# Performance work log

Hardware: AMD Instinct MI355X
Metric: run time of the kernel (lower is better)

## Reference

```python
import jax, jax.numpy as jnp
import numpy as np

N = 50000
E = 600000
D_IN = 128
D_OUT = 128
EPS = 1e-12  # F.normalize eps


def setup_inputs() -> dict:
    key = jax.random.key(0)
    ks = jax.random.split(key, 10)
    s = 1.0 / np.sqrt(D_IN)
    inp = {
        "x": jax.random.normal(ks[0], (N, D_IN), dtype=jnp.float32),
        "edge_index": jax.random.randint(ks[1], (2, E), 0, N, dtype=jnp.int64),
        # conv1: lin_l (with bias) applied to aggregated neighbors, lin_r (no bias) to root
        "W1l": jax.random.uniform(ks[2], (D_IN, D_IN), jnp.float32, -s, s),
        "b1": jax.random.uniform(ks[3], (D_IN,), jnp.float32, -s, s),
        "W1r": jax.random.uniform(ks[4], (D_IN, D_IN), jnp.float32, -s, s),
        # conv2
        "W2l": jax.random.uniform(ks[5], (D_IN, D_OUT), jnp.float32, -s, s),
        "b2": jax.random.uniform(ks[6], (D_OUT,), jnp.float32, -s, s),
        "W2r": jax.random.uniform(ks[7], (D_IN, D_OUT), jnp.float32, -s, s),
        # final fc
        "Wf": jax.random.uniform(ks[8], (D_OUT, D_OUT), jnp.float32, -s, s),
        "bf": jax.random.uniform(ks[9], (D_OUT,), jnp.float32, -s, s),
    }
    return inp


def _sage_conv(x, src, dst, Wl, bl, Wr):
    # mean-aggregate messages from source nodes onto destination nodes
    msgs = x[src]  # [E, d] gather
    agg = jax.ops.segment_sum(msgs, dst, num_segments=N)  # [N, d]
    cnt = jax.ops.segment_sum(jnp.ones((src.shape[0],), x.dtype), dst, num_segments=N)
    agg = agg / jnp.maximum(cnt, 1.0)[:, None]  # isolated nodes -> 0
    out = agg @ Wl + bl + x @ Wr
    # L2 normalize per node (PyG normalize=True)
    nrm = jnp.sqrt(jnp.sum(out * out, axis=-1, keepdims=True))
    return out / jnp.maximum(nrm, EPS)


def reference(x, edge_index, W1l, b1, W1r, W2l, b2, W2r, Wf, bf):
    src, dst = edge_index[0], edge_index[1]
    h = jax.nn.relu(_sage_conv(x, src, dst, W1l, b1, W1r))
    h = jax.nn.relu(_sage_conv(h, src, dst, W2l, b2, W2r))
    return h @ Wf + bf
```

## Files before the change

kernel.cpp:

```cpp
#include <hip/hip_runtime.h>
#include <hip/hip_fp16.h>

#define D 128
#define SCAN_B 256
#define HLD 136

typedef __attribute__((ext_vector_type(8))) _Float16 f16x8;
typedef __attribute__((ext_vector_type(4))) float f32x4;

__global__ void count_kernel(const int* __restrict__ ei, int E, int* __restrict__ cnt) {
    int t = blockIdx.x * blockDim.x + threadIdx.x;
    if (t < E) atomicAdd(&cnt[ei[E + t]], 1);
}

__global__ void scan_pass1(const int* __restrict__ cnt, int* __restrict__ rs,
                           int* __restrict__ bsum, int N) {
    __shared__ int lds[SCAN_B];
    int tid = threadIdx.x;
    int i = blockIdx.x * SCAN_B + tid;
    int v = (i < N) ? cnt[i] : 0;
    lds[tid] = v;
    __syncthreads();
    for (int o = 1; o < SCAN_B; o <<= 1) {
        int t = (tid >= o) ? lds[tid - o] : 0;
        __syncthreads();
        lds[tid] += t;
        __syncthreads();
    }
    if (i < N) rs[i] = lds[tid] - v;
    if (tid == SCAN_B - 1) bsum[blockIdx.x] = lds[tid];
}

__global__ void scan_pass2(int* __restrict__ bsum, int nb) {
    __shared__ int lds[SCAN_B];
    int tid = threadIdx.x;
    int v = (tid < nb) ? bsum[tid] : 0;
    lds[tid] = v;
    __syncthreads();
    for (int o = 1; o < SCAN_B; o <<= 1) {
        int t = (tid >= o) ? lds[tid - o] : 0;
        __syncthreads();
        lds[tid] += t;
        __syncthreads();
    }
    if (tid < nb) bsum[tid] = lds[tid] - v;
}

__global__ void scan_pass3(int* __restrict__ rs, int* __restrict__ cursor,
                           const int* __restrict__ bsum, const int* __restrict__ cnt,
                           float* __restrict__ inv, int N) {
    int i = blockIdx.x * SCAN_B + threadIdx.x;
    if (i < N) {
        int v = rs[i] + bsum[blockIdx.x];
        rs[i] = v;
        cursor[i] = v;
        inv[i] = 1.0f / (float)max(cnt[i], 1);
    }
}

__global__ void fill_kernel(const int* __restrict__ ei, int E,
                            int* __restrict__ cursor, int* __restrict__ csr) {
    int e = blockIdx.x * blockDim.x + threadIdx.x;
    if (e < E) {
        int src = ei[e], dst = ei[E + e];
        int pos = atomicAdd(&cursor[dst], 1);
        csr[pos] = src;
    }
}

__global__ void cvt_half_kernel(const float* __restrict__ x, __half* __restrict__ xh, int n8) {
    int i = blockIdx.x * blockDim.x + threadIdx.x;
    if (i >= n8) return;
    const float4* x4 = (const float4*)x;
    float4 a = x4[2 * i], b = x4[2 * i + 1];
    __half2 h0 = __floats2half2_rn(a.x, a.y);
    __half2 h1 = __floats2half2_rn(a.z, a.w);
    __half2 h2 = __floats2half2_rn(b.x, b.y);
    __half2 h3 = __floats2half2_rn(b.z, b.w);
    uint4 o;
    o.x = *(const unsigned*)&h0;
    o.y = *(const unsigned*)&h1;
    o.z = *(const unsigned*)&h2;
    o.w = *(const unsigned*)&h3;
    ((uint4*)xh)[i] = o;
}

__device__ __forceinline__ void acc8(uint4 v, float* s) {
    const __half2* h = reinterpret_cast<const __half2*>(&v);
    float2 f0 = __half22float2(h[0]);
    float2 f1 = __half22float2(h[1]);
    float2 f2 = __half22float2(h[2]);
    float2 f3 = __half22float2(h[3]);
    s[0] += f0.x; s[1] += f0.y; s[2] += f1.x; s[3] += f1.y;
    s[4] += f2.x; s[5] += f2.y; s[6] += f3.x; s[7] += f3.y;
}

__global__ void aggregate_kernel(const __half* __restrict__ xh, int sstride,
                                 const int* __restrict__ csr,
                                 const int* __restrict__ rs, const int* __restrict__ cnt,
                                 const float* __restrict__ inv,
                                 __half* __restrict__ aggh, __half* __restrict__ aggl, int N) {
    int t = blockIdx.x * blockDim.x + threadIdx.x;
    int node = t >> 4;
    int c = t & 15;
    if (node >= N) return;
    int deg = cnt[node];
    int st = rs[node];
    const uint4* x4 = (const uint4*)xh;
    float s[8] = {0.f, 0.f, 0.f, 0.f, 0.f, 0.f, 0.f, 0.f};
    int i = 0;
    for (; i + 4 <= deg; i += 4) {
        int n0 = csr[st + i + 0], n1 = csr[st + i + 1];
        int n2 = csr[st + i + 2], n3 = csr[st + i + 3];
        uint4 v0 = x4[(size_t)n0 * sstride + c];
        uint4 v1 = x4[(size_t)n1 * sstride + c];
        uint4 v2 = x4[(size_t)n2 * sstride + c];
        uint4 v3 = x4[(size_t)n3 * sstride + c];
        acc8(v0, s); acc8(v1, s); acc8(v2, s); acc8(v3, s);
    }
    for (; i < deg; i++) {
        int n0 = csr[st + i];
        uint4 v0 = x4[(size_t)n0 * sstride + c];
        acc8(v0, s);
    }
    float iv = inv[node];
    uint4 oh, ol;
    __half2* ph = (__half2*)&oh;
    __half2* pl = (__half2*)&ol;
#pragma unroll
    for (int jj = 0; jj < 4; jj++) {
        float v0 = s[2 * jj] * iv, v1 = s[2 * jj + 1] * iv;
        __half h0 = __float2half_rn(v0), h1 = __float2half_rn(v1);
        ph[jj] = __halves2half2(h0, h1);
        pl[jj] = __halves2half2(__float2half_rn(v0 - __half2float(h0)),
                                __float2half_rn(v1 - __half2float(h1)));
    }
    ((uint4*)aggh)[(size_t)node * 16 + c] = oh;
    ((uint4*)aggl)[(size_t)node * 16 + c] = ol;
}

__global__ void pack_kernel(const float* __restrict__ W1l, const float* __restrict__ W1r,
                            const float* __restrict__ W2l, const float* __restrict__ W2r,
                            const float* __restrict__ Wf, unsigned short* __restrict__ pw) {
    int idx = blockIdx.x * blockDim.x + threadIdx.x;
    if (idx >= 5 * 2048) return;
    int w = idx >> 11;
    int r = idx & 2047;
    int ks = r >> 9;
    int t = (r >> 6) & 7;
    int lane = r & 63;
    int q = lane >> 4, n = lane & 15;
    const float* W = (w == 0) ? W1l : (w == 1) ? W1r : (w == 2) ? W2l : (w == 3) ? W2r : Wf;
    unsigned short* dh = pw + (size_t)w * 32768;
    unsigned short* dl = dh + 16384;
    int off = ((ks * 8 + t) * 64 + lane) * 8;
#pragma unroll
    for (int j = 0; j < 8; j++) {
        float v = W[(size_t)(ks * 32 + q * 8 + j) * D + t * 16 + n];
        __half hb = __float2half_rn(v);
        dh[off + j] = __half_as_ushort(hb);
        dl[off + j] = __half_as_ushort(__float2half_rn(v - __half2float(hb)));
    }
}

__device__ __forceinline__ void split_f16(const float* v, uint4& hi, uint4& lo) {
    __half2* ph = (__half2*)&hi;
    __half2* pl = (__half2*)&lo;
#pragma unroll
    for (int jj = 0; jj < 4; jj++) {
        __half h0 = __float2half_rn(v[2 * jj]);
        __half h1 = __float2half_rn(v[2 * jj + 1]);
        ph[jj] = __halves2half2(h0, h1);
        pl[jj] = __halves2half2(__float2half_rn(v[2 * jj] - __half2float(h0)),
                                __float2half_rn(v[2 * jj + 1] - __half2float(h1)));
    }
}

template <int LAYER>
__global__ __launch_bounds__(256) void mfma_gemm(
        const uint4* __restrict__ Agh, const uint4* __restrict__ Agl,
        const float* __restrict__ Xf,
        const uint4* Hio,
        const uint4* __restrict__ W0h, const uint4* __restrict__ W0l,
        const uint4* __restrict__ W1h, const uint4* __restrict__ W1l,
        const float* __restrict__ bias,
        const uint4* __restrict__ W2h, const uint4* __restrict__ W2l,
        const float* __restrict__ bias2,
        float* out, __half* Hout, int N) {
    __shared__ __half Hs[(LAYER == 2) ? 4 * 2 * 16 * HLD : 4];

    const int tid = threadIdx.x;
    const int lane = tid & 63;
    const int wave = tid >> 6;
    const int c = lane & 15;
    const int q = lane >> 4;
    const int R = blockIdx.x * 64 + wave * 16;
    int row0 = R + c;
    if (row0 >= N) row0 = N - 1;

    uint4 Ah_[8], Al_[8];
    const size_t rb16 = (size_t)row0 * 16 + q;
#pragma unroll
    for (int kl = 0; kl < 4; kl++) {
        Ah_[kl] = Agh[rb16 + kl * 4];
        Al_[kl] = Agl[rb16 + kl * 4];
    }
    if (LAYER == 1) {
        const float4* xf4 = (const float4*)Xf;
        const size_t xb = (size_t)row0 * 32 + q * 2;
        float4 xa[8];
#pragma unroll
        for (int kl = 0; kl < 4; kl++) {
            xa[2 * kl] = xf4[xb + kl * 8];
            xa[2 * kl + 1] = xf4[xb + kl * 8 + 1];
        }
#pragma unroll
        for (int kl = 0; kl < 4; kl++) {
            float v[8] = {xa[2 * kl].x, xa[2 * kl].y, xa[2 * kl].z, xa[2 * kl].w,
                          xa[2 * kl + 1].x, xa[2 * kl + 1].y, xa[2 * kl + 1].z, xa[2 * kl + 1].w};
            split_f16(v, Ah_[4 + kl], Al_[4 + kl]);
        }
    } else {
        const size_t rb32 = (size_t)row0 * 32 + q;
#pragma unroll
        for (int kl = 0; kl < 4; kl++) {
            Ah_[4 + kl] = Hio[rb32 + kl * 4];
            Al_[4 + kl] = Hio[rb32 + 16 + kl * 4];
        }
    }

    f32x4 acc[8];
#pragma unroll
    for (int t = 0; t < 8; t++)
#pragma unroll
        for (int r = 0; r < 4; r++) acc[t][r] = 0.0f;

#pragma unroll
    for (int ks = 0; ks < 8; ks++) {
        const uint4* Wh = ((ks < 4) ? W0h : W1h) + (size_t)(ks & 3) * 512 + lane;
        const uint4* Wl = ((ks < 4) ? W0l : W1l) + (size_t)(ks & 3) * 512 + lane;
        f16x8 ah = __builtin_bit_cast(f16x8, Ah_[ks]);
        f16x8 al = __builtin_bit_cast(f16x8, Al_[ks]);
#pragma unroll
        for (int t = 0; t < 8; t++) {
            f16x8 bh = __builtin_bit_cast(f16x8, Wh[t * 64]);
            f16x8 bl = __builtin_bit_cast(f16x8, Wl[t * 64]);
            acc[t] = __builtin_amdgcn_mfma_f32_16x16x32_f16(ah, bh, acc[t], 0, 0, 0);
            acc[t] = __builtin_amdgcn_mfma_f32_16x16x32_f16(al, bh, acc[t], 0, 0, 0);
            acc[t] = __builtin_amdgcn_mfma_f32_16x16x32_f16(ah, bl, acc[t], 0, 0, 0);
        }
    }

#pragma unroll
    for (int t = 0; t < 8; t++) {
        float bv = bias[t * 16 + c];
#pragma unroll
        for (int r = 0; r < 4; r++) acc[t][r] += bv;
    }
#pragma unroll
    for (int r = 0; r < 4; r++) {
        float v = 0.0f;
#pragma unroll
        for (int t = 0; t < 8; t++) v += acc[t][r] * acc[t][r];
        v += __shfl_xor(v, 1, 16);
        v += __shfl_xor(v, 2, 16);
        v += __shfl_xor(v, 4, 16);
        v += __shfl_xor(v, 8, 16);
        float rn = 1.0f / fmaxf(sqrtf(v), 1e-12f);
#pragma unroll
        for (int t = 0; t < 8; t++) acc[t][r] = fmaxf(acc[t][r] * rn, 0.0f);
    }

    if (LAYER == 1) {
#pragma unroll
        for (int t = 0; t < 8; t++)
#pragma unroll
            for (int r = 0; r < 4; r++) {
                int row = R + q * 4 + r;
                if (row < N) {
                    float v = acc[t][r];
                    __half h = __float2half_rn(v);
                    size_t base = (size_t)row * 256;
                    Hout[base + t * 16 + c] = h;
                    Hout[base + 128 + t * 16 + c] = __float2half_rn(v - __half2float(h));
                }
            }
        return;
    }

    __half* hh = &Hs[wave * (2 * 16 * HLD)];
    __half* hl = hh + 16 * HLD;
#pragma unroll
    for (int t = 0; t < 8; t++)
#pragma unroll
        for (int r = 0; r < 4; r++) {
            int m = q * 4 + r;
            float v = acc[t][r];
            __half h = __float2half_rn(v);
            hh[m * HLD + t * 16 + c] = h;
            hl[m * HLD + t * 16 + c] = __float2half_rn(v - __half2float(h));
        }
    __syncthreads();

    uint4 a2h_[4], a2l_[4];
#pragma unroll
    for (int k2 = 0; k2 < 4; k2++) {
        a2h_[k2] = *(const uint4*)&hh[c * HLD + k2 * 32 + q * 8];
        a2l_[k2] = *(const uint4*)&hl[c * HLD + k2 * 32 + q * 8];
    }

    f32x4 acc2[8];
#pragma unroll
    for (int t = 0; t < 8; t++) {
        float bv = bias2[t * 16 + c];
#pragma unroll
        for (int r = 0; r < 4; r++) acc2[t][r] = bv;
    }
#pragma unroll
    for (int k2 = 0; k2 < 4; k2++) {
        const uint4* Wh = W2h + (size_t)k2 * 512 + lane;
        const uint4* Wl = W2l + (size_t)k2 * 512 + lane;
        f16x8 ah = __builtin_bit_cast(f16x8, a2h_[k2]);
        f16x8 al = __builtin_bit_cast(f16x8, a2l_[k2]);
#pragma unroll
        for (int t = 0; t < 8; t++) {
            f16x8 bh = __builtin_bit_cast(f16x8, Wh[t * 64]);
            f16x8 bl = __builtin_bit_cast(f16x8, Wl[t * 64]);
            acc2[t] = __builtin_amdgcn_mfma_f32_16x16x32_f16(ah, bh, acc2[t], 0, 0, 0);
            acc2[t] = __builtin_amdgcn_mfma_f32_16x16x32_f16(al, bh, acc2[t], 0, 0, 0);
            acc2[t] = __builtin_amdgcn_mfma_f32_16x16x32_f16(ah, bl, acc2[t], 0, 0, 0);
        }
    }

#pragma unroll
    for (int t = 0; t < 8; t++)
#pragma unroll
        for (int r = 0; r < 4; r++) {
            int row = R + q * 4 + r;
            if (row < N) out[(size_t)row * D + t * 16 + c] = acc2[t][r];
        }
}

extern "C" void kernel_launch(void* const* d_in, const int* in_sizes, int n_in,
                              void* d_out, int out_size, void* d_ws, size_t ws_size,
                              hipStream_t stream) {
    const float* x   = (const float*)d_in[0];
    const int*   ei  = (const int*)d_in[1];
    const float* W1l = (const float*)d_in[2];
    const float* b1  = (const float*)d_in[3];
    const float* W1r = (const float*)d_in[4];
    const float* W2l = (const float*)d_in[5];
    const float* b2  = (const float*)d_in[6];
    const float* W2r = (const float*)d_in[7];
    const float* Wf  = (const float*)d_in[8];
    const float* bf  = (const float*)d_in[9];
    float* out = (float*)d_out;

    int N = in_sizes[0] / D;
    int E = in_sizes[1] / 2;

    __half* Agh = (__half*)d_ws;
    __half* Agl = Agh + (size_t)N * D;
    __half* Xh  = Agl + (size_t)N * D;
    float* inv  = (float*)(Xh + (size_t)N * D);
    int*   rs     = (int*)(inv + N);
    int*   cnt    = rs + N;
    int*   cursor = cnt + N;
    int*   bsum   = cursor + N;
    int*   csr    = bsum + 256;
    unsigned short* pw = (unsigned short*)(csr + E);
    unsigned short* p1lh = pw + 0 * 32768, *p1ll = p1lh + 16384;
    unsigned short* p1rh = pw + 1 * 32768, *p1rl = p1rh + 16384;
    unsigned short* p2lh = pw + 2 * 32768, *p2ll = p2lh + 16384;
    unsigned short* p2rh = pw + 3 * 32768, *p2rl = p2rh + 16384;
    unsigned short* pfh  = pw + 4 * 32768, *pfl  = pfh + 16384;

    __half* H1 = (__half*)d_out;

    int nb = (N + SCAN_B - 1) / SCAN_B;

    hipMemsetAsync(cnt, 0, (size_t)N * sizeof(int), stream);
    pack_kernel<<<40, 256, 0, stream>>>(W1l, W1r, W2l, W2r, Wf, pw);
    int n8 = N * 16;
    cvt_half_kernel<<<(n8 + 255) / 256, 256, 0, stream>>>(x, Xh, n8);
    count_kernel<<<(E + 255) / 256, 256, 0, stream>>>(ei, E, cnt);
    scan_pass1<<<nb, SCAN_B, 0, stream>>>(cnt, rs, bsum, N);
    scan_pass2<<<1, SCAN_B, 0, stream>>>(bsum, nb);
    scan_pass3<<<nb, SCAN_B, 0, stream>>>(rs, cursor, bsum, cnt, inv, N);
    fill_kernel<<<(E + 255) / 256, 256, 0, stream>>>(ei, E, cursor, csr);

    int agg_blocks = (N * 16 + 255) / 256;
    int gemm_blocks = (N + 63) / 64;

    aggregate_kernel<<<agg_blocks, 256, 0, stream>>>(Xh, 16, csr, rs, cnt, inv, Agh, Agl, N);
    mfma_gemm<1><<<gemm_blocks, 256, 0, stream>>>(
        (const uint4*)Agh, (const uint4*)Agl, x, nullptr,
        (const uint4*)p1lh, (const uint4*)p1ll, (const uint4*)p1rh, (const uint4*)p1rl, b1,
        nullptr, nullptr, nullptr, nullptr, H1, N);

    aggregate_kernel<<<agg_blocks, 256, 0, stream>>>(H1, 32, csr, rs, cnt, inv, Agh, Agl, N);
    mfma_gemm<2><<<gemm_blocks, 256, 0, stream>>>(
        (const uint4*)Agh, (const uint4*)Agl, nullptr, (const uint4*)d_out,
        (const uint4*)p2lh, (const uint4*)p2ll, (const uint4*)p2rh, (const uint4*)p2rl, b2,
        (const uint4*)pfh, (const uint4*)pfl, bf, out, nullptr, N);
}
```

Baseline: 280.5 us.

## Fuse prologue kernels and process two row tiles per wave in MFMA GEMM

Merges weight packing, x-to-half conversion and in-degree counting into one prologue launch, which removes two kernel launches and their serialization gaps. The GEMM kernels now have each wave compute two 16-row tiles, so every weight fragment loaded from global memory feeds twice as many MFMAs, and the grid is halved. The cost is roughly double the register use for the A fragments and accumulators; launch_bounds(256,2) caps registers to keep occupancy and may cause spills. Layer 2 also reuses the shared-memory staging buffer once per tile, which adds barriers.

```diff
diff --git a/kernel.cpp b/kernel.cpp
--- a/kernel.cpp
+++ b/kernel.cpp
@@ -7,11 +7,6 @@
 
 typedef __attribute__((ext_vector_type(8))) _Float16 f16x8;
 typedef __attribute__((ext_vector_type(4))) float f32x4;
-
-__global__ void count_kernel(const int* __restrict__ ei, int E, int* __restrict__ cnt) {
-    int t = blockIdx.x * blockDim.x + threadIdx.x;
-    if (t < E) atomicAdd(&cnt[ei[E + t]], 1);
-}
 
 __global__ void scan_pass1(const int* __restrict__ cnt, int* __restrict__ rs,
                            int* __restrict__ bsum, int N) {
@@ -68,21 +63,49 @@
     }
 }
 
-__global__ void cvt_half_kernel(const float* __restrict__ x, __half* __restrict__ xh, int n8) {
-    int i = blockIdx.x * blockDim.x + threadIdx.x;
-    if (i >= n8) return;
-    const float4* x4 = (const float4*)x;
-    float4 a = x4[2 * i], b = x4[2 * i + 1];
-    __half2 h0 = __floats2half2_rn(a.x, a.y);
-    __half2 h1 = __floats2half2_rn(a.z, a.w);
-    __half2 h2 = __floats2half2_rn(b.x, b.y);
-    __half2 h3 = __floats2half2_rn(b.z, b.w);
-    uint4 o;
-    o.x = *(const unsigned*)&h0;
-    o.y = *(const unsigned*)&h1;
-    o.z = *(const unsigned*)&h2;
-    o.w = *(const unsigned*)&h3;
-    ((uint4*)xh)[i] = o;
+__global__ void prologue_kernel(const float* __restrict__ W1l, const float* __restrict__ W1r,
+                                const float* __restrict__ W2l, const float* __restrict__ W2r,
+                                const float* __restrict__ Wf, unsigned short* __restrict__ pw,
+                                const float* __restrict__ x, __half* __restrict__ xh, int n8,
+                                const int* __restrict__ ei, int E, int* __restrict__ cnt) {
+    int t = blockIdx.x * blockDim.x + threadIdx.x;
+    if (t < 10240) {
+        int idx = t;
+        int w = idx >> 11;
+        int r = idx & 2047;
+        int ks = r >> 9;
+        int tt = (r >> 6) & 7;
+        int lane = r & 63;
+        int q = lane >> 4, n = lane & 15;
+        const float* W = (w == 0) ? W1l : (w == 1) ? W1r : (w == 2) ? W2l : (w == 3) ? W2r : Wf;
+        unsigned short* dh = pw + (size_t)w * 32768;
+        unsigned short* dl = dh + 16384;
+        int off = ((ks * 8 + tt) * 64 + lane) * 8;
+#pragma unroll
+        for (int j = 0; j < 8; j++) {
+            float v = W[(size_t)(ks * 32 + q * 8 + j) * D + tt * 16 + n];
+            __half hb = __float2half_rn(v);
+            dh[off + j] = __half_as_ushort(hb);
+            dl[off + j] = __half_as_ushort(__float2half_rn(v - __half2float(hb)));
+        }
+    } else if (t < 10240 + n8) {
+        int i = t - 10240;
+        const float4* x4 = (const float4*)x;
+        float4 a = x4[2 * i], b = x4[2 * i + 1];
+        __half2 h0 = __floats2half2_rn(a.x, a.y);
+        __half2 h1 = __floats2half2_rn(a.z, a.w);
+        __half2 h2 = __floats2half2_rn(b.x, b.y);
+        __half2 h3 = __floats2half2_rn(b.z, b.w);
+        uint4 o;
+        o.x = *(const unsigned*)&h0;
+        o.y = *(const unsigned*)&h1;
+        o.z = *(const unsigned*)&h2;
+        o.w = *(const unsigned*)&h3;
+        ((uint4*)xh)[i] = o;
+    } else {
+        int e = t - 10240 - n8;
+        if (e < E) atomicAdd(&cnt[ei[E + e]], 1);
+    }
 }
 
 __device__ __forceinline__ void acc8(uint4 v, float* s) {
@@ -139,30 +162,6 @@
     ((uint4*)aggl)[(size_t)node * 16 + c] = ol;
 }
 
-__global__ void pack_kernel(const float* __restrict__ W1l, const float* __restrict__ W1r,
-                            const float* __restrict__ W2l, const float* __restrict__ W2r,
-                            const float* __restrict__ Wf, unsigned short* __restrict__ pw) {
-    int idx = blockIdx.x * blockDim.x + threadIdx.x;
-    if (idx >= 5 * 2048) return;
-    int w = idx >> 11;
-    int r = idx & 2047;
-    int ks = r >> 9;
-    int t = (r >> 6) & 7;
-    int lane = r & 63;
-    int q = lane >> 4, n = lane & 15;
-    const float* W = (w == 0) ? W1l : (w == 1) ? W1r : (w == 2) ? W2l : (w == 3) ? W2r : Wf;
-    unsigned short* dh = pw + (size_t)w * 32768;
-    unsigned short* dl = dh + 16384;
-    int off = ((ks * 8 + t) * 64 + lane) * 8;
-#pragma unroll
-    for (int j = 0; j < 8; j++) {
-        float v = W[(size_t)(ks * 32 + q * 8 + j) * D + t * 16 + n];
-        __half hb = __float2half_rn(v);
-        dh[off + j] = __half_as_ushort(hb);
-        dl[off + j] = __half_as_ushort(__float2half_rn(v - __half2float(hb)));
-    }
-}
-
 __device__ __forceinline__ void split_f16(const float* v, uint4& hi, uint4& lo) {
     __half2* ph = (__half2*)&hi;
     __half2* pl = (__half2*)&lo;
@@ -177,7 +176,7 @@
 }
 
 template <int LAYER>
-__global__ __launch_bounds__(256) void mfma_gemm(
+__global__ __launch_bounds__(256, 2) void mfma_gemm(
         const uint4* __restrict__ Agh, const uint4* __restrict__ Agl,
         const float* __restrict__ Xf,
         const uint4* Hio,
@@ -194,151 +193,175 @@
     const int wave = tid >> 6;
     const int c = lane & 15;
     const int q = lane >> 4;
-    const int R = blockIdx.x * 64 + wave * 16;
-    int row0 = R + c;
-    if (row0 >= N) row0 = N - 1;
-
-    uint4 Ah_[8], Al_[8];
-    const size_t rb16 = (size_t)row0 * 16 + q;
-#pragma unroll
-    for (int kl = 0; kl < 4; kl++) {
-        Ah_[kl] = Agh[rb16 + kl * 4];
-        Al_[kl] = Agl[rb16 + kl * 4];
-    }
-    if (LAYER == 1) {
-        const float4* xf4 = (const float4*)Xf;
-        const size_t xb = (size_t)row0 * 32 + q * 2;
-        float4 xa[8];
+    const int R = blockIdx.x * 128 + wave * 32;
+
+    int rowA[2];
+    rowA[0] = min(R + c, N - 1);
+    rowA[1] = min(R + 16 + c, N - 1);
+
+    uint4 Ah_[2][8], Al_[2][8];
+#pragma unroll
+    for (int tile = 0; tile < 2; tile++) {
+        const size_t rb16 = (size_t)rowA[tile] * 16 + q;
 #pragma unroll
         for (int kl = 0; kl < 4; kl++) {
-            xa[2 * kl] = xf4[xb + kl * 8];
-            xa[2 * kl + 1] = xf4[xb + kl * 8 + 1];
-        }
-#pragma unroll
-        for (int kl = 0; kl < 4; kl++) {
-            float v[8] = {xa[2 * kl].x, xa[2 * kl].y, xa[2 * kl].z, xa[2 * kl].w,
-                          xa[2 * kl + 1].x, xa[2 * kl + 1].y, xa[2 * kl + 1].z, xa[2 * kl + 1].w};
-            split_f16(v, Ah_[4 + kl], Al_[4 + kl]);
-        }
-    } else {
-        const size_t rb32 = (size_t)row0 * 32 + q;
-#pragma unroll
-        for (int kl = 0; kl < 4; kl++) {
-            Ah_[4 + kl] = Hio[rb32 + kl * 4];
-            Al_[4 + kl] = Hio[rb32 + 16 + kl * 4];
-        }
-    }
-
-    f32x4 acc[8];
-#pragma unroll
-    for (int t = 0; t < 8; t++)
-#pragma unroll
-        for (int r = 0; r < 4; r++) acc[t][r] = 0.0f;
+            Ah_[tile][kl] = Agh[rb16 + kl * 4];
+            Al_[tile][kl] = Agl[rb16 + kl * 4];
+        }
+        if (LAYER == 1) {
+            const float4* xf4 = (const float4*)Xf;
+            const size_t xb = (size_t)rowA[tile] * 32 + q * 2;
+#pragma unroll
+            for (int kl = 0; kl < 4; kl++) {
+                float4 xa = xf4[xb + kl * 8];
+                float4 xbv = xf4[xb + kl * 8 + 1];
+                float v[8] = {xa.x, xa.y, xa.z, xa.w, xbv.x, xbv.y, xbv.z, xbv.w};
+                split_f16(v, Ah_[tile][4 + kl], Al_[tile][4 + kl]);
+            }
+        } else {
+            const size_t rb32 = (size_t)rowA[tile] * 32 + q;
+#pragma unroll
+            for (int kl = 0; kl < 4; kl++) {
+                Ah_[tile][4 + kl] = Hio[rb32 + kl * 4];
+                Al_[tile][4 + kl] = Hio[rb32 + 16 + kl * 4];
+            }
+        }
+    }
+
+    f32x4 acc[2][8];
+#pragma unroll
+    for (int tile = 0; tile < 2; tile++)
+#pragma unroll
+        for (int t = 0; t < 8; t++)
+#pragma unroll
+            for (int r = 0; r < 4; r++) acc[tile][t][r] = 0.0f;
 
 #pragma unroll
     for (int ks = 0; ks < 8; ks++) {
         const uint4* Wh = ((ks < 4) ? W0h : W1h) + (size_t)(ks & 3) * 512 + lane;
         const uint4* Wl = ((ks < 4) ? W0l : W1l) + (size_t)(ks & 3) * 512 + lane;
-        f16x8 ah = __builtin_bit_cast(f16x8, Ah_[ks]);
-        f16x8 al = __builtin_bit_cast(f16x8, Al_[ks]);
+        f16x8 a0h = __builtin_bit_cast(f16x8, Ah_[0][ks]);
+        f16x8 a0l = __builtin_bit_cast(f16x8, Al_[0][ks]);
+        f16x8 a1h = __builtin_bit_cast(f16x8, Ah_[1][ks]);
+        f16x8 a1l = __builtin_bit_cast(f16x8, Al_[1][ks]);
 #pragma unroll
         for (int t = 0; t < 8; t++) {
             f16x8 bh = __builtin_bit_cast(f16x8, Wh[t * 64]);
             f16x8 bl = __builtin_bit_cast(f16x8, Wl[t * 64]);
-            acc[t] = __builtin_amdgcn_mfma_f32_16x16x32_f16(ah, bh, acc[t], 0, 0, 0);
-            acc[t] = __builtin_amdgcn_mfma_f32_16x16x32_f16(al, bh, acc[t], 0, 0, 0);
-            acc[t] = __builtin_amdgcn_mfma_f32_16x16x32_f16(ah, bl, acc[t], 0, 0, 0);
-        }
-    }
-
-#pragma unroll
-    for (int t = 0; t < 8; t++) {
-        float bv = bias[t * 16 + c];
-#pragma unroll
-        for (int r = 0; r < 4; r++) acc[t][r] += bv;
-    }
-#pragma unroll
-    for (int r = 0; r < 4; r++) {
-        float v = 0.0f;
-#pragma unroll
-        for (int t = 0; t < 8; t++) v += acc[t][r] * acc[t][r];
-        v += __shfl_xor(v, 1, 16);
-        v += __shfl_xor(v, 2, 16);
-        v += __shfl_xor(v, 4, 16);
-        v += __shfl_xor(v, 8, 16);
-        float rn = 1.0f / fmaxf(sqrtf(v), 1e-12f);
-#pragma unroll
-        for (int t = 0; t < 8; t++) acc[t][r] = fmaxf(acc[t][r] * rn, 0.0f);
+            acc[0][t] = __builtin_amdgcn_mfma_f32_16x16x32_f16(a0h, bh, acc[0][t], 0, 0, 0);
+            acc[0][t] = __builtin_amdgcn_mfma_f32_16x16x32_f16(a0l, bh, acc[0][t], 0, 0, 0);
+            acc[0][t] = __builtin_amdgcn_mfma_f32_16x16x32_f16(a0h, bl, acc[0][t], 0, 0, 0);
+            acc[1][t] = __builtin_amdgcn_mfma_f32_16x16x32_f16(a1h, bh, acc[1][t], 0, 0, 0);
+            acc[1][t] = __builtin_amdgcn_mfma_f32_16x16x32_f16(a1l, bh, acc[1][t], 0, 0, 0);
+            acc[1][t] = __builtin_amdgcn_mfma_f32_16x16x32_f16(a1h, bl, acc[1][t], 0, 0, 0);
+        }
+    }
+
+#pragma unroll
+    for (int tile = 0; tile < 2; tile++) {
+#pragma unroll
+        for (int t = 0; t < 8; t++) {
+            float bv = bias[t * 16 + c];
+#pragma unroll
+            for (int r = 0; r < 4; r++) acc[tile][t][r] += bv;
+        }
+#pragma unroll
+        for (int r = 0; r < 4; r++) {
+            float v = 0.0f;
+#pragma unroll
+            for (int t = 0; t < 8; t++) v += acc[tile][t][r] * acc[tile][t][r];
+            v += __shfl_xor(v, 1, 16);
+            v += __shfl_xor(v, 2, 16);
+            v += __shfl_xor(v, 4, 16);
+            v += __shfl_xor(v, 8, 16);
+            float rn = 1.0f / fmaxf(sqrtf(v), 1e-12f);
+#pragma unroll
+            for (int t = 0; t < 8; t++) acc[tile][t][r] = fmaxf(acc[tile][t][r] * rn, 0.0f);
+        }
     }
 
     if (LAYER == 1) {
 #pragma unroll
-        for (int t = 0; t < 8; t++)
-#pragma unroll
-            for (int r = 0; r < 4; r++) {
-                int row = R + q * 4 + r;
-                if (row < N) {
-                    float v = acc[t][r];
-                    __half h = __float2half_rn(v);
-                    size_t base = (size_t)row * 256;
-                    Hout[base + t * 16 + c] = h;
-                    Hout[base + 128 + t * 16 + c] = __float2half_rn(v - __half2float(h));
+        for (int tile = 0; tile < 2; tile++)
+#pragma unroll
+            for (int t = 0; t < 8; t++)
+#pragma unroll
+                for (int r = 0; r < 4; r++) {
+                    int row = R + tile * 16 + q * 4 + r;
+                    if (row < N) {
+                        float v = acc[tile][t][r];
+                        __half h = __float2half_rn(v);
+                        size_t base = (size_t)row * 256;
+                        Hout[base + t * 16 + c] = h;
+                        Hout[base + 128 + t * 16 + c] = __float2half_rn(v - __half2float(h));
+                    }
                 }
-            }
         return;
     }
 
     __half* hh = &Hs[wave * (2 * 16 * HLD)];
     __half* hl = hh + 16 * HLD;
-#pragma unroll
-    for (int t = 0; t < 8; t++)
-#pragma unroll
-        for (int r = 0; r < 4; r++) {
-            int m = q * 4 + r;
-            float v = acc[t][r];
-            __half h = __float2half_rn(v);
-            hh[m * HLD + t * 16 + c] = h;
-            hl[m * HLD + t * 16 + c] = __float2half_rn(v - __half2float(h));
-        }
-    __syncthreads();
-
-    uint4 a2h_[4], a2l_[4];
-#pragma unroll
-    for (int k2 = 0; k2 < 4; k2++) {
-        a2h_[k2] = *(const uint4*)&hh[c * HLD + k2 * 32 + q * 8];
-        a2l_[k2] = *(const uint4*)&hl[c * HLD + k2 * 32 + q * 8];
-    }
-
-    f32x4 acc2[8];
-#pragma unroll
-    for (int t = 0; t < 8; t++) {
-        float bv = bias2[t * 16 + c];
-#pragma unroll
-        for (int r = 0; r < 4; r++) acc2[t][r] = bv;
-    }
+    uint4 a2h_[2][4], a2l_[2][4];
+#pragma unroll
+    for (int tile = 0; tile < 2; tile++) {
+        __syncthreads();
+#pragma unroll
+        for (int t = 0; t < 8; t++)
+#pragma unroll
+            for (int r = 0; r < 4; r++) {
+                int m = q * 4 + r;
+                float v = acc[tile][t][r];
+                __half h = __float2half_rn(v);
+                hh[m * HLD + t * 16 + c] = h;
+                hl[m * HLD + t * 16 + c] = __float2half_rn(v - __half2float(h));
+            }
+        __syncthreads();
+#pragma unroll
+        for (int k2 = 0; k2 < 4; k2++) {
+            a2h_[tile][k2] = *(const uint4*)&hh[c * HLD + k2 * 32 + q * 8];
+            a2l_[tile][k2] = *(const uint4*)&hl[c * HLD + k2 * 32 + q * 8];
+        }
+    }
+
+    f32x4 acc2[2][8];
+#pragma unroll
+    for (int tile = 0; tile < 2; tile++)
+#pragma unroll
+        for (int t = 0; t < 8; t++) {
+            float bv = bias2[t * 16 + c];
+#pragma unroll
+            for (int r = 0; r < 4; r++) acc2[tile][t][r] = bv;
+        }
 #pragma unroll
     for (int k2 = 0; k2 < 4; k2++) {
         const uint4* Wh = W2h + (size_t)k2 * 512 + lane;
         const uint4* Wl = W2l + (size_t)k2 * 512 + lane;
-        f16x8 ah = __builtin_bit_cast(f16x8, a2h_[k2]);
-        f16x8 al = __builtin_bit_cast(f16x8, a2l_[k2]);
+        f16x8 a0h = __builtin_bit_cast(f16x8, a2h_[0][k2]);
+        f16x8 a0l = __builtin_bit_cast(f16x8, a2l_[0][k2]);
+        f16x8 a1h = __builtin_bit_cast(f16x8, a2h_[1][k2]);
+        f16x8 a1l = __builtin_bit_cast(f16x8, a2l_[1][k2]);
 #pragma unroll
         for (int t = 0; t < 8; t++) {
             f16x8 bh = __builtin_bit_cast(f16x8, Wh[t * 64]);
             f16x8 bl = __builtin_bit_cast(f16x8, Wl[t * 64]);
-            acc2[t] = __builtin_amdgcn_mfma_f32_16x16x32_f16(ah, bh, acc2[t], 0, 0, 0);
-            acc2[t] = __builtin_amdgcn_mfma_f32_16x16x32_f16(al, bh, acc2[t], 0, 0, 0);
-            acc2[t] = __builtin_amdgcn_mfma_f32_16x16x32_f16(ah, bl, acc2[t], 0, 0, 0);
-        }
-    }
-
-#pragma unroll
-    for (int t = 0; t < 8; t++)
-#pragma unroll
-        for (int r = 0; r < 4; r++) {
-            int row = R + q * 4 + r;
-            if (row < N) out[(size_t)row * D + t * 16 + c] = acc2[t][r];
-        }
+            acc2[0][t] = __builtin_amdgcn_mfma_f32_16x16x32_f16(a0h, bh, acc2[0][t], 0, 0, 0);
+            acc2[0][t] = __builtin_amdgcn_mfma_f32_16x16x32_f16(a0l, bh, acc2[0][t], 0, 0, 0);
+            acc2[0][t] = __builtin_amdgcn_mfma_f32_16x16x32_f16(a0h, bl, acc2[0][t], 0, 0, 0);
+            acc2[1][t] = __builtin_amdgcn_mfma_f32_16x16x32_f16(a1h, bh, acc2[1][t], 0, 0, 0);
+            acc2[1][t] = __builtin_amdgcn_mfma_f32_16x16x32_f16(a1l, bh, acc2[1][t], 0, 0, 0);
+            acc2[1][t] = __builtin_amdgcn_mfma_f32_16x16x32_f16(a1h, bl, acc2[1][t], 0, 0, 0);
+        }
+    }
+
+#pragma unroll
+    for (int tile = 0; tile < 2; tile++)
+#pragma unroll
+        for (int t = 0; t < 8; t++)
+#pragma unroll
+            for (int r = 0; r < 4; r++) {
+                int row = R + tile * 16 + q * 4 + r;
+                if (row < N) out[(size_t)row * D + t * 16 + c] = acc2[tile][t][r];
+            }
 }
 
 extern "C" void kernel_launch(void* const* d_in, const int* in_sizes, int n_in,
@@ -378,19 +401,19 @@
     __half* H1 = (__half*)d_out;
 
     int nb = (N + SCAN_B - 1) / SCAN_B;
+    int n8 = N * 16;
 
     hipMemsetAsync(cnt, 0, (size_t)N * sizeof(int), stream);
-    pack_kernel<<<40, 256, 0, stream>>>(W1l, W1r, W2l, W2r, Wf, pw);
-    int n8 = N * 16;
-    cvt_half_kernel<<<(n8 + 255) / 256, 256, 0, stream>>>(x, Xh, n8);
-    count_kernel<<<(E + 255) / 256, 256, 0, stream>>>(ei, E, cnt);
+    int pro_threads = 10240 + n8 + E;
+    prologue_kernel<<<(pro_threads + 255) / 256, 256, 0, stream>>>(
+        W1l, W1r, W2l, W2r, Wf, pw, x, Xh, n8, ei, E, cnt);
     scan_pass1<<<nb, SCAN_B, 0, stream>>>(cnt, rs, bsum, N);
     scan_pass2<<<1, SCAN_B, 0, stream>>>(bsum, nb);
     scan_pass3<<<nb, SCAN_B, 0, stream>>>(rs, cursor, bsum, cnt, inv, N);
     fill_kernel<<<(E + 255) / 256, 256, 0, stream>>>(ei, E, cursor, csr);
 
     int agg_blocks = (N * 16 + 255) / 256;
-    int gemm_blocks = (N + 63) / 64;
+    int gemm_blocks = (N + 127) / 128;
 
     aggregate_kernel<<<agg_blocks, 256, 0, stream>>>(Xh, 16, csr, rs, cnt, inv, Agh, Agl, N);
     mfma_gemm<1><<<gemm_blocks, 256, 0, stream>>>(
```

Result: slower. 291.3 us (+3.8%).

## Fuse prologue kernels into one launch and double-buffer weight loads in GEMM

Applied to the files above, without the earlier changes.

Merges the weight packing, fp16 conversion of x and in-degree counting kernels into a single launch that partitions threads by index range, removing two kernel launches and their serialization gaps. Separately, both GEMM loops now prefetch the next K-slice of packed weights into a register double buffer before issuing the MFMAs for the current slice, aiming to hide global/L2 load latency behind matrix math. The prefetch raises register pressure (32 extra uint4 per buffer pair), which may reduce occupancy or cause spills.

```diff
diff --git a/kernel.cpp b/kernel.cpp
--- a/kernel.cpp
+++ b/kernel.cpp
@@ -7,11 +7,6 @@
 
 typedef __attribute__((ext_vector_type(8))) _Float16 f16x8;
 typedef __attribute__((ext_vector_type(4))) float f32x4;
-
-__global__ void count_kernel(const int* __restrict__ ei, int E, int* __restrict__ cnt) {
-    int t = blockIdx.x * blockDim.x + threadIdx.x;
-    if (t < E) atomicAdd(&cnt[ei[E + t]], 1);
-}
 
 __global__ void scan_pass1(const int* __restrict__ cnt, int* __restrict__ rs,
                            int* __restrict__ bsum, int N) {
@@ -68,21 +63,49 @@
     }
 }
 
-__global__ void cvt_half_kernel(const float* __restrict__ x, __half* __restrict__ xh, int n8) {
-    int i = blockIdx.x * blockDim.x + threadIdx.x;
-    if (i >= n8) return;
-    const float4* x4 = (const float4*)x;
-    float4 a = x4[2 * i], b = x4[2 * i + 1];
-    __half2 h0 = __floats2half2_rn(a.x, a.y);
-    __half2 h1 = __floats2half2_rn(a.z, a.w);
-    __half2 h2 = __floats2half2_rn(b.x, b.y);
-    __half2 h3 = __floats2half2_rn(b.z, b.w);
-    uint4 o;
-    o.x = *(const unsigned*)&h0;
-    o.y = *(const unsigned*)&h1;
-    o.z = *(const unsigned*)&h2;
-    o.w = *(const unsigned*)&h3;
-    ((uint4*)xh)[i] = o;
+__global__ void prologue_kernel(const float* __restrict__ W1l, const float* __restrict__ W1r,
+                                const float* __restrict__ W2l, const float* __restrict__ W2r,
+                                const float* __restrict__ Wf, unsigned short* __restrict__ pw,
+                                const float* __restrict__ x, __half* __restrict__ xh, int n8,
+                                const int* __restrict__ ei, int E, int* __restrict__ cnt) {
+    int t = blockIdx.x * blockDim.x + threadIdx.x;
+    if (t < 10240) {
+        int idx = t;
+        int w = idx >> 11;
+        int r = idx & 2047;
+        int ks = r >> 9;
+        int tt = (r >> 6) & 7;
+        int lane = r & 63;
+        int q = lane >> 4, n = lane & 15;
+        const float* W = (w == 0) ? W1l : (w == 1) ? W1r : (w == 2) ? W2l : (w == 3) ? W2r : Wf;
+        unsigned short* dh = pw + (size_t)w * 32768;
+        unsigned short* dl = dh + 16384;
+        int off = ((ks * 8 + tt) * 64 + lane) * 8;
+#pragma unroll
+        for (int j = 0; j < 8; j++) {
+            float v = W[(size_t)(ks * 32 + q * 8 + j) * D + tt * 16 + n];
+            __half hb = __float2half_rn(v);
+            dh[off + j] = __half_as_ushort(hb);
+            dl[off + j] = __half_as_ushort(__float2half_rn(v - __half2float(hb)));
+        }
+    } else if (t < 10240 + n8) {
+        int i = t - 10240;
+        const float4* x4 = (const float4*)x;
+        float4 a = x4[2 * i], b = x4[2 * i + 1];
+        __half2 h0 = __floats2half2_rn(a.x, a.y);
+        __half2 h1 = __floats2half2_rn(a.z, a.w);
+        __half2 h2 = __floats2half2_rn(b.x, b.y);
+        __half2 h3 = __floats2half2_rn(b.z, b.w);
+        uint4 o;
+        o.x = *(const unsigned*)&h0;
+        o.y = *(const unsigned*)&h1;
+        o.z = *(const unsigned*)&h2;
+        o.w = *(const unsigned*)&h3;
+        ((uint4*)xh)[i] = o;
+    } else {
+        int e = t - 10240 - n8;
+        if (e < E) atomicAdd(&cnt[ei[E + e]], 1);
+    }
 }
 
 __device__ __forceinline__ void acc8(uint4 v, float* s) {
@@ -139,30 +162,6 @@
     ((uint4*)aggl)[(size_t)node * 16 + c] = ol;
 }
 
-__global__ void pack_kernel(const float* __restrict__ W1l, const float* __restrict__ W1r,
-                            const float* __restrict__ W2l, const float* __restrict__ W2r,
-                            const float* __restrict__ Wf, unsigned short* __restrict__ pw) {
-    int idx = blockIdx.x * blockDim.x + threadIdx.x;
-    if (idx >= 5 * 2048) return;
-    int w = idx >> 11;
-    int r = idx & 2047;
-    int ks = r >> 9;
-    int t = (r >> 6) & 7;
-    int lane = r & 63;
-    int q = lane >> 4, n = lane & 15;
-    const float* W = (w == 0) ? W1l : (w == 1) ? W1r : (w == 2) ? W2l : (w == 3) ? W2r : Wf;
-    unsigned short* dh = pw + (size_t)w * 32768;
-    unsigned short* dl = dh + 16384;
-    int off = ((ks * 8 + t) * 64 + lane) * 8;
-#pragma unroll
-    for (int j = 0; j < 8; j++) {
-        float v = W[(size_t)(ks * 32 + q * 8 + j) * D + t * 16 + n];
-        __half hb = __float2half_rn(v);
-        dh[off + j] = __half_as_ushort(hb);
-        dl[off + j] = __half_as_ushort(__float2half_rn(v - __half2float(hb)));
-    }
-}
-
 __device__ __forceinline__ void split_f16(const float* v, uint4& hi, uint4& lo) {
     __half2* ph = (__half2*)&hi;
     __half2* pl = (__half2*)&lo;
@@ -195,8 +194,7 @@
     const int c = lane & 15;
     const int q = lane >> 4;
     const int R = blockIdx.x * 64 + wave * 16;
-    int row0 = R + c;
-    if (row0 >= N) row0 = N - 1;
+    const int row0 = min(R + c, N - 1);
 
     uint4 Ah_[8], Al_[8];
     const size_t rb16 = (size_t)row0 * 16 + q;
@@ -229,6 +227,13 @@
         }
     }
 
+    uint4 wh[2][8], wl[2][8];
+#pragma unroll
+    for (int t = 0; t < 8; t++) {
+        wh[0][t] = W0h[(size_t)t * 64 + lane];
+        wl[0][t] = W0l[(size_t)t * 64 + lane];
+    }
+
     f32x4 acc[8];
 #pragma unroll
     for (int t = 0; t < 8; t++)
@@ -237,14 +242,21 @@
 
 #pragma unroll
     for (int ks = 0; ks < 8; ks++) {
-        const uint4* Wh = ((ks < 4) ? W0h : W1h) + (size_t)(ks & 3) * 512 + lane;
-        const uint4* Wl = ((ks < 4) ? W0l : W1l) + (size_t)(ks & 3) * 512 + lane;
+        if (ks < 7) {
+            const uint4* Whn = (((ks + 1) < 4) ? W0h : W1h) + (size_t)((ks + 1) & 3) * 512 + lane;
+            const uint4* Wln = (((ks + 1) < 4) ? W0l : W1l) + (size_t)((ks + 1) & 3) * 512 + lane;
+#pragma unroll
+            for (int t = 0; t < 8; t++) {
+                wh[(ks + 1) & 1][t] = Whn[t * 64];
+                wl[(ks + 1) & 1][t] = Wln[t * 64];
+            }
+        }
         f16x8 ah = __builtin_bit_cast(f16x8, Ah_[ks]);
         f16x8 al = __builtin_bit_cast(f16x8, Al_[ks]);
 #pragma unroll
         for (int t = 0; t < 8; t++) {
-            f16x8 bh = __builtin_bit_cast(f16x8, Wh[t * 64]);
-            f16x8 bl = __builtin_bit_cast(f16x8, Wl[t * 64]);
+            f16x8 bh = __builtin_bit_cast(f16x8, wh[ks & 1][t]);
+            f16x8 bl = __builtin_bit_cast(f16x8, wl[ks & 1][t]);
             acc[t] = __builtin_amdgcn_mfma_f32_16x16x32_f16(ah, bh, acc[t], 0, 0, 0);
             acc[t] = __builtin_amdgcn_mfma_f32_16x16x32_f16(al, bh, acc[t], 0, 0, 0);
             acc[t] = __builtin_amdgcn_mfma_f32_16x16x32_f16(ah, bl, acc[t], 0, 0, 0);
@@ -288,6 +300,13 @@
         return;
     }
 
+    uint4 w2h[2][8], w2l[2][8];
+#pragma unroll
+    for (int t = 0; t < 8; t++) {
+        w2h[0][t] = W2h[(size_t)t * 64 + lane];
+        w2l[0][t] = W2l[(size_t)t * 64 + lane];
+    }
+
     __half* hh = &Hs[wave * (2 * 16 * HLD)];
     __half* hl = hh + 16 * HLD;
 #pragma unroll
@@ -318,14 +337,21 @@
     }
 #pragma unroll
     for (int k2 = 0; k2 < 4; k2++) {
-        const uint4* Wh = W2h + (size_t)k2 * 512 + lane;
-        const uint4* Wl = W2l + (size_t)k2 * 512 + lane;
+        if (k2 < 3) {
+            const uint4* Whn = W2h + (size_t)(k2 + 1) * 512 + lane;
+            const uint4* Wln = W2l + (size_t)(k2 + 1) * 512 + lane;
+#pragma unroll
+            for (int t = 0; t < 8; t++) {
+                w2h[(k2 + 1) & 1][t] = Whn[t * 64];
+                w2l[(k2 + 1) & 1][t] = Wln[t * 64];
+            }
+        }
         f16x8 ah = __builtin_bit_cast(f16x8, a2h_[k2]);
         f16x8 al = __builtin_bit_cast(f16x8, a2l_[k2]);
 #pragma unroll
         for (int t = 0; t < 8; t++) {
-            f16x8 bh = __builtin_bit_cast(f16x8, Wh[t * 64]);
-            f16x8 bl = __builtin_bit_cast(f16x8, Wl[t * 64]);
+            f16x8 bh = __builtin_bit_cast(f16x8, w2h[k2 & 1][t]);
+            f16x8 bl = __builtin_bit_cast(f16x8, w2l[k2 & 1][t]);
             acc2[t] = __builtin_amdgcn_mfma_f32_16x16x32_f16(ah, bh, acc2[t], 0, 0, 0);
             acc2[t] = __builtin_amdgcn_mfma_f32_16x16x32_f16(al, bh, acc2[t], 0, 0, 0);
             acc2[t] = __builtin_amdgcn_mfma_f32_16x16x32_f16(ah, bl, acc2[t], 0, 0, 0);
@@ -378,12 +404,12 @@
     __half* H1 = (__half*)d_out;
 
     int nb = (N + SCAN_B - 1) / SCAN_B;
+    int n8 = N * 16;
 
     hipMemsetAsync(cnt, 0, (size_t)N * sizeof(int), stream);
-    pack_kernel<<<40, 256, 0, stream>>>(W1l, W1r, W2l, W2r, Wf, pw);
-    int n8 = N * 16;
-    cvt_half_kernel<<<(n8 + 255) / 256, 256, 0, stream>>>(x, Xh, n8);
-    count_kernel<<<(E + 255) / 256, 256, 0, stream>>>(ei, E, cnt);
+    int pro_threads = 10240 + n8 + E;
+    prologue_kernel<<<(pro_threads + 255) / 256, 256, 0, stream>>>(
+        W1l, W1r, W2l, W2r, Wf, pw, x, Xh, n8, ei, E, cnt);
     scan_pass1<<<nb, SCAN_B, 0, stream>>>(cnt, rs, bsum, N);
     scan_pass2<<<1, SCAN_B, 0, stream>>>(bsum, nb);
     scan_pass3<<<nb, SCAN_B, 0, stream>>>(rs, cursor, bsum, cnt, inv, N);
```

Result: slower. 287.3 us (+2.4%).
